# Optimization experiments

Hardware: AMD Instinct MI355X
Metric: run time of the kernel (lower is better)

## Reference

```python
import jax, jax.numpy as jnp
import numpy as np

B, N, D, H, WIN = 8, 4096, 768, 8, 8
HD = D // H
FG = N // 2 + 1
FL = WIN // 2 + 1


def _gelu(x):
    return jax.nn.gelu(x, approximate=False)


def _cgelu(z):
    # magnitude-based complex GELU: z * gelu(|z|) / (|z| + 1e-6)
    mag = jnp.abs(z)
    return z * (_gelu(mag) / (mag + 1e-6))


def setup_inputs():
    key = jax.random.key(0)
    ks = jax.random.split(key, 8)

    def w(k, shape):
        return jax.random.normal(k, shape, dtype=jnp.float32) * 0.02

    return {
        "x": jax.random.normal(ks[0], (B, N, D), dtype=jnp.float32),
        "ln_w": jnp.ones((D,), jnp.float32),
        "ln_b": jnp.zeros((D,), jnp.float32),
        "bf_g": jnp.ones((H, FG, 1), jnp.float32),
        "bb_g": jnp.full((H, FG, 1), -0.1, jnp.float32),
        "bf_l": jnp.ones((H, FL, 1), jnp.float32),
        "bb_l": jnp.full((H, FL, 1), -0.1, jnp.float32),
        "w1g": w(ks[1], (D, D)),
        "b1g": jnp.zeros((D,), jnp.float32),
        "w2g": w(ks[2], (D, H * FG * 2)),
        "b2g": jnp.zeros((H * FG * 2,), jnp.float32),
        "w1l": w(ks[3], (D, D)),
        "b1l": jnp.zeros((D,), jnp.float32),
        "w2l": w(ks[4], (D, H * FL * 2)),
        "b2l": jnp.zeros((H * FL * 2,), jnp.float32),
        "wf1": w(ks[5], (D, D // 2)),
        "bf1": jnp.zeros((D // 2,), jnp.float32),
        "wf2": w(ks[6], (D // 2, H)),
        "bf2": jnp.zeros((H,), jnp.float32),
    }


def reference(x, ln_w, ln_b, bf_g, bb_g, bf_l, bb_l, w1g, b1g, w2g, b2g,
              w1l, b1l, w2l, b2l, wf1, bf1, wf2, bf2):
    # pre-norm (LayerNorm, eps=1e-5)
    mu = jnp.mean(x, axis=-1, keepdims=True)
    var = jnp.mean((x - mu) ** 2, axis=-1, keepdims=True)
    xn = (x - mu) / jnp.sqrt(var + 1e-5) * ln_w + ln_b
    xh = xn.reshape(B, N, H, HD).transpose(0, 2, 1, 3)  # (B,H,N,HD)
    ctx = xn.mean(axis=1)  # (B,D)

    # ---- global branch: Hann-windowed rFFT over full sequence ----
    ag = (_gelu(ctx @ w1g + b1g) @ w2g + b2g).reshape(B, H, FG, 2)
    hann_g = jnp.hanning(N).astype(x.dtype)[None, None, :, None]
    Ff = jnp.fft.rfft(xh * hann_g, axis=2, norm="ortho")  # (B,H,FG,HD) complex
    eff_f = bf_g[None] * (1.0 + ag[..., 0:1])
    eff_b = bb_g[None] + ag[..., 1:2]
    x_global = jnp.fft.irfft(_cgelu(Ff * eff_f + eff_b), n=N, axis=2, norm="ortho")

    al = (_gelu(ctx @ w1l + b1l) @ w2l + b2l).reshape(B, H, FL, 2)
    nw = N // WIN
    hann_l = jnp.hanning(WIN).astype(x.dtype)[None, None, None, :, None]
    xw = xh.reshape(B, H, nw, WIN, HD) * hann_l
    Fl_fft = jnp.fft.rfft(xw, axis=3, norm="ortho")  # (B,H,nw,FL,HD)
    eff_fl = bf_l[None, :, None] * (1.0 + al[:, :, None, :, 0:1])
    eff_bl = bb_l[None, :, None] + al[:, :, None, :, 1:2]
    x_local = jnp.fft.irfft(_cgelu(Fl_fft * eff_fl + eff_bl), n=WIN, axis=3,
                            norm="ortho").reshape(B, H, N, HD)

    # ---- fusion gate ----
    alpha = jax.nn.sigmoid(_gelu(ctx @ wf1 + bf1) @ wf2 + bf2).reshape(B, H, 1, 1)
    fused = alpha * x_global + (1.0 - alpha) * x_local
    return x + fused.transpose(0, 2, 1, 3).reshape(B, N, D)
```

## Files before the change

### kernel.cpp

```cpp
#include <hip/hip_runtime.h>
#include <math.h>

#define B_ 8
#define N_ 4096
#define D_ 768
#define H_ 8
#define HD_ 96
#define FG_ 2049
#define TWO_PI 6.283185307179586476925f
#define PAD(i) ((i) + ((i) >> 5))

__device__ __forceinline__ float gelu_f(float x) {
    return 0.5f * x * (1.0f + erff(x * 0.7071067811865475f));
}

__global__ void k_init(const float* __restrict__ b2g, const float* __restrict__ b2l,
                       float2* __restrict__ twg, float* __restrict__ hanng,
                       float* __restrict__ ctx, float* __restrict__ ag,
                       float* __restrict__ al) {
    int i = blockIdx.x * 256 + threadIdx.x;
    if (i < 2048) {
        float s, c;
        sincosf(-TWO_PI * (float)i / 4096.0f, &s, &c);
        twg[i] = make_float2(c, s);
    }
    if (i < 4096) hanng[i] = 0.5f - 0.5f * cosf(TWO_PI * (float)i / 4095.0f);
    if (i < B_ * D_) ctx[i] = 0.f;
    const int CG = H_ * FG_ * 2;
    if (i < CG) {
        float v = b2g[i];
        for (int b = 0; b < B_; ++b) ag[(size_t)b * CG + i] = v;
    } else if (i < CG + 80) {
        int cc = i - CG;
        float v = b2l[cc];
        for (int b = 0; b < B_; ++b) al[b * 80 + cc] = v;
    }
}

__global__ __launch_bounds__(256) void k_stats(const float* __restrict__ x,
                                               float* __restrict__ mu,
                                               float* __restrict__ rstd) {
    int row = blockIdx.x * 4 + (threadIdx.x >> 6);
    int lane = threadIdx.x & 63;
    const float4* xr = (const float4*)(x + (size_t)row * D_);
    float4 a = xr[lane], b = xr[lane + 64], c = xr[lane + 128];
    float s = a.x + a.y + a.z + a.w + b.x + b.y + b.z + b.w + c.x + c.y + c.z + c.w;
    #pragma unroll
    for (int o = 32; o > 0; o >>= 1) s += __shfl_xor(s, o);
    float m = s * (1.0f / 768.0f);
    float v = 0.f, d;
    d = a.x - m; v += d * d; d = a.y - m; v += d * d;
    d = a.z - m; v += d * d; d = a.w - m; v += d * d;
    d = b.x - m; v += d * d; d = b.y - m; v += d * d;
    d = b.z - m; v += d * d; d = b.w - m; v += d * d;
    d = c.x - m; v += d * d; d = c.y - m; v += d * d;
    d = c.z - m; v += d * d; d = c.w - m; v += d * d;
    #pragma unroll
    for (int o = 32; o > 0; o >>= 1) v += __shfl_xor(v, o);
    if (lane == 0) {
        mu[row] = m;
        rstd[row] = rsqrtf(v * (1.0f / 768.0f) + 1e-5f);
    }
}

__global__ __launch_bounds__(256) void k_lnT(const float* __restrict__ x,
                                             const float* __restrict__ mu,
                                             const float* __restrict__ rstd,
                                             const float* __restrict__ lw,
                                             const float* __restrict__ lb,
                                             float* __restrict__ xt,
                                             float* __restrict__ ctx) {
    __shared__ float tile[64][65];
    __shared__ float csum[4][64];
    int d0 = blockIdx.x * 64, n0 = blockIdx.y * 64, b = blockIdx.z;
    int c = threadIdx.x & 63, r4 = threadIdx.x >> 6;
    float w = lw[d0 + c], bias = lb[d0 + c];
    float partial = 0.f;
    #pragma unroll
    for (int q = 0; q < 16; ++q) {
        int r = r4 * 16 + q;
        int row = b * N_ + n0 + r;
        float v = (x[(size_t)row * D_ + d0 + c] - mu[row]) * rstd[row] * w + bias;
        tile[r][c] = v;
        partial += v;
    }
    csum[r4][c] = partial;
    __syncthreads();
    if (r4 == 0)
        atomicAdd(ctx + b * D_ + d0 + c,
                  (csum[0][c] + csum[1][c] + csum[2][c] + csum[3][c]) * (1.0f / 4096.0f));
    #pragma unroll
    for (int q = 0; q < 16; ++q) {
        int r = r4 * 16 + q;
        xt[((size_t)b * D_ + d0 + r) * N_ + n0 + c] = tile[c][r];
    }
}

__global__ void k_mlp1(const float* __restrict__ ctx,
                       const float* __restrict__ w1g, const float* __restrict__ b1g,
                       const float* __restrict__ w1l, const float* __restrict__ b1l,
                       const float* __restrict__ wf1, const float* __restrict__ bf1,
                       float* __restrict__ h1g, float* __restrict__ h1l, float* __restrict__ hf) {
    __shared__ float cl[B_ * D_];
    for (int i = threadIdx.x; i < B_ * D_; i += 256) cl[i] = ctx[i];
    __syncthreads();
    int c = blockIdx.x * 256 + threadIdx.x;
    if (c >= 1920) return;
    const float *w, *bias; float* out; int ncol, cc;
    if (c < 768)      { w = w1g; bias = b1g; out = h1g; ncol = 768; cc = c; }
    else if (c < 1536){ w = w1l; bias = b1l; out = h1l; ncol = 768; cc = c - 768; }
    else              { w = wf1; bias = bf1; out = hf;  ncol = 384; cc = c - 1536; }
    float acc[B_];
    #pragma unroll
    for (int b = 0; b < B_; ++b) acc[b] = 0.f;
    for (int d = 0; d < 768; ++d) {
        float wv = w[(size_t)d * ncol + cc];
        #pragma unroll
        for (int b = 0; b < B_; ++b) acc[b] += cl[b * 768 + d] * wv;
    }
    float bv = bias[cc];
    for (int b = 0; b < B_; ++b) out[b * ncol + cc] = gelu_f(acc[b] + bv);
}

__global__ void k_mlp2(const float* __restrict__ h1g, const float* __restrict__ h1l,
                       const float* __restrict__ hf,
                       const float* __restrict__ w2g, const float* __restrict__ w2l,
                       const float* __restrict__ wf2, const float* __restrict__ bf2,
                       float* __restrict__ ag, float* __restrict__ al, float* __restrict__ gate) {
    int kc = blockIdx.y;
    int d0 = kc * 96;
    __shared__ float lg[B_ * 96];
    __shared__ float ll[B_ * 96];
    for (int i = threadIdx.x; i < B_ * 96; i += 256) {
        int bb = i / 96, dd = i % 96;
        lg[i] = h1g[bb * 768 + d0 + dd];
        ll[i] = h1l[bb * 768 + d0 + dd];
    }
    __syncthreads();
    int c = blockIdx.x * 256 + threadIdx.x;
    const int CG = H_ * FG_ * 2;
    float acc[B_];
    #pragma unroll
    for (int b = 0; b < B_; ++b) acc[b] = 0.f;
    if (c < CG) {
        for (int d = 0; d < 96; ++d) {
            float wv = w2g[(size_t)(d0 + d) * CG + c];
            #pragma unroll
            for (int b = 0; b < B_; ++b) acc[b] += lg[b * 96 + d] * wv;
        }
        for (int b = 0; b < B_; ++b) atomicAdd(ag + (size_t)b * CG + c, acc[b]);
    } else if (c < CG + 80) {
        int cc = c - CG;
        for (int d = 0; d < 96; ++d) {
            float wv = w2l[(d0 + d) * 80 + cc];
            #pragma unroll
            for (int b = 0; b < B_; ++b) acc[b] += ll[b * 96 + d] * wv;
        }
        for (int b = 0; b < B_; ++b) atomicAdd(al + b * 80 + cc, acc[b]);
    } else if (c < CG + 88 && kc == 0) {
        int cc = c - CG - 80;
        for (int d = 0; d < 384; ++d) {
            float wv = wf2[d * 8 + cc];
            #pragma unroll
            for (int b = 0; b < B_; ++b) acc[b] += hf[b * 384 + d] * wv;
        }
        for (int b = 0; b < B_; ++b)
            gate[b * 8 + cc] = 1.0f / (1.0f + expf(-(acc[b] + bf2[cc])));
    }
}

__device__ __forceinline__ void fft_pass(float2* z, const float2* tw4,
                                         const float2* __restrict__ twg,
                                         int t, float sign) {
    float2 v[16];
    #pragma unroll
    for (int i = 0; i < 16; ++i) v[i] = z[PAD(t * 16 + i)];
    const float TC[8] = {1.f, 0.92387953251f, 0.70710678119f, 0.38268343236f,
                         0.f, -0.38268343236f, -0.70710678119f, -0.92387953251f};
    const float TS[8] = {0.f, -0.38268343236f, -0.70710678119f, -0.92387953251f,
                         -1.f, -0.92387953251f, -0.70710678119f, -0.38268343236f};
    #pragma unroll
    for (int s = 1; s <= 4; ++s) {
        int half = 1 << (s - 1);
        #pragma unroll
        for (int u = 0; u < 8; ++u) {
            int lg = u >> (s - 1), pos = u & (half - 1);
            int i1 = (lg << s) + pos, i2 = i1 + half;
            int m = pos << (4 - s);
            float wr = TC[m], wi = sign * TS[m];
            float2 a = v[i1], bb = v[i2];
            float tr = bb.x * wr - bb.y * wi;
            float ti = bb.x * wi + bb.y * wr;
            v[i1] = make_float2(a.x + tr, a.y + ti);
            v[i2] = make_float2(a.x - tr, a.y - ti);
        }
    }
    #pragma unroll
    for (int i = 0; i < 16; ++i) z[PAD(t * 16 + i)] = v[i];
    __syncthreads();
    for (int s = 5; s <= 10; ++s) {
        int half = 1 << (s - 1);
        int sh = 12 - s;
        #pragma unroll
        for (int u = 0; u < 8; ++u) {
            int j = t + (u << 8);
            int grp = j >> (s - 1);
            int pos = j & (half - 1);
            int i1 = (grp << s) + pos;
            int p1 = PAD(i1), p2 = PAD(i1 + half);
            float2 w = tw4[PAD(pos << (sh - 2))];
            float wi = sign * w.y;
            float2 a = z[p1], bb = z[p2];
            float tr = bb.x * w.x - bb.y * wi;
            float ti = bb.x * wi + bb.y * w.x;
            z[p1] = make_float2(a.x + tr, a.y + ti);
            z[p2] = make_float2(a.x - tr, a.y - ti);
        }
        __syncthreads();
    }
    for (int s = 11; s <= 12; ++s) {
        int half = 1 << (s - 1);
        int sh = 12 - s;
        #pragma unroll
        for (int u = 0; u < 8; ++u) {
            int j = t + (u << 8);
            int grp = j >> (s - 1);
            int pos = j & (half - 1);
            int i1 = (grp << s) + pos;
            int p1 = PAD(i1), p2 = PAD(i1 + half);
            float2 w = twg[pos << sh];
            float wi = sign * w.y;
            float2 a = z[p1], bb = z[p2];
            float tr = bb.x * w.x - bb.y * wi;
            float ti = bb.x * wi + bb.y * w.x;
            z[p1] = make_float2(a.x + tr, a.y + ti);
            z[p2] = make_float2(a.x - tr, a.y - ti);
        }
        __syncthreads();
    }
}

__global__ __launch_bounds__(256) void k_spectral(
        const float* __restrict__ xt,
        const float* __restrict__ ag,
        const float* __restrict__ al,
        const float* __restrict__ gate,
        const float* __restrict__ bf_g, const float* __restrict__ bb_g,
        const float* __restrict__ bf_l, const float* __restrict__ bb_l,
        const float2* __restrict__ twg, const float* __restrict__ hanng,
        float* __restrict__ fused)
{
    __shared__ float2 z[4224];
    __shared__ float2 tw4[528];
    int line0 = blockIdx.x * 2;
    int d0 = line0 % 768, b = line0 / 768;
    int h = d0 / HD_;
    int t = threadIdx.x;

    for (int m = t; m < 512; m += 256) tw4[PAD(m)] = twg[4 * m];

    const float* src0 = xt + (size_t)line0 * N_;
    const float* src1 = src0 + N_;
    float raw0[16], raw1[16];
    #pragma unroll
    for (int q = 0; q < 4; ++q) {
        float4 v0 = ((const float4*)src0)[t * 4 + q];
        float4 v1 = ((const float4*)src1)[t * 4 + q];
        raw0[q * 4 + 0] = v0.x; raw0[q * 4 + 1] = v0.y;
        raw0[q * 4 + 2] = v0.z; raw0[q * 4 + 3] = v0.w;
        raw1[q * 4 + 0] = v1.x; raw1[q * 4 + 1] = v1.y;
        raw1[q * 4 + 2] = v1.z; raw1[q * 4 + 3] = v1.w;
    }
    #pragma unroll
    for (int q = 0; q < 4; ++q) {
        float4 hw = ((const float4*)hanng)[t * 4 + q];
        int nb = t * 16 + q * 4;
        int r0 = PAD((int)(__brev((unsigned)(nb + 0)) >> 20));
        int r1 = PAD((int)(__brev((unsigned)(nb + 1)) >> 20));
        int r2 = PAD((int)(__brev((unsigned)(nb + 2)) >> 20));
        int r3 = PAD((int)(__brev((unsigned)(nb + 3)) >> 20));
        z[r0] = make_float2(raw0[q * 4 + 0] * hw.x, raw1[q * 4 + 0] * hw.x);
        z[r1] = make_float2(raw0[q * 4 + 1] * hw.y, raw1[q * 4 + 1] * hw.y);
        z[r2] = make_float2(raw0[q * 4 + 2] * hw.z, raw1[q * 4 + 2] * hw.z);
        z[r3] = make_float2(raw0[q * 4 + 3] * hw.w, raw1[q * 4 + 3] * hw.w);
    }

    float alc = gate[b * 8 + h];
    const float* alb = al + b * 80;
    float effl_f[5], effl_b[5];
    #pragma unroll
    for (int f = 0; f < 5; ++f) {
        int idx = h * 5 + f;
        effl_f[f] = bf_l[idx] * (1.0f + alb[idx * 2]);
        effl_b[f] = bb_l[idx] + alb[idx * 2 + 1];
    }
    const float s8 = 0.3535533905932738f;
    const float c7 = 0.7071067811865476f;
    const float cosT[8] = {1.f, c7, 0.f, -c7, -1.f, -c7, 0.f, c7};
    const float sinT[8] = {0.f, c7, 1.f, c7, 0.f, -c7, -1.f, -c7};
    const float hl[8] = {0.f, 0.18825510f, 0.61126047f, 0.95048444f,
                         0.95048444f, 0.61126047f, 0.18825510f, 0.f};
    float xl0[16], xl1[16];
    #pragma unroll
    for (int ln = 0; ln < 2; ++ln) {
        float* rawp = ln ? raw1 : raw0;
        float* xlp  = ln ? xl1 : xl0;
        #pragma unroll
        for (int w2 = 0; w2 < 2; ++w2) {
            float xw[8];
            #pragma unroll
            for (int j = 0; j < 8; ++j) xw[j] = rawp[w2 * 8 + j] * hl[j];
            float Yr[5], Yi[5];
            #pragma unroll
            for (int f = 0; f < 5; ++f) {
                float fr = 0.f, fi = 0.f;
                #pragma unroll
                for (int j = 0; j < 8; ++j) {
                    int k8 = (f * j) & 7;
                    fr += xw[j] * cosT[k8];
                    fi -= xw[j] * sinT[k8];
                }
                fr *= s8; fi *= s8;
                float zr = fr * effl_f[f] + effl_b[f];
                float zi = fi * effl_f[f];
                float mag = sqrtf(zr * zr + zi * zi);
                float g = gelu_f(mag) / (mag + 1e-6f);
                Yr[f] = zr * g; Yi[f] = zi * g;
            }
            #pragma unroll
            for (int j = 0; j < 8; ++j) {
                float acc = Yr[0] + Yr[4] * ((j & 1) ? -1.f : 1.f);
                #pragma unroll
                for (int f = 1; f < 4; ++f) {
                    int k8 = (f * j) & 7;
                    acc += 2.f * (Yr[f] * cosT[k8] - Yi[f] * sinT[k8]);
                }
                xlp[w2 * 8 + j] = acc * s8;
            }
        }
    }

    __syncthreads();
    fft_pass(z, tw4, twg, t, 1.0f);

    const float inv64 = 1.0f / 64.0f;
    const float* agb = ag + (size_t)b * 32784;
    for (int k = t; k < 2048; k += 256) {
        int km = (4096 - k) & 4095;
        int pk = PAD(k), pm = PAD(km);
        float2 Z = z[pk], Z2 = z[pm];
        float X0r = 0.5f * (Z.x + Z2.x), X0i = 0.5f * (Z.y - Z2.y);
        float X1r = 0.5f * (Z.y + Z2.y), X1i = -0.5f * (Z.x - Z2.x);
        int idx = h * FG_ + k;
        float efff = bf_g[idx] * (1.0f + agb[idx * 2]);
        float effb = bb_g[idx] + agb[idx * 2 + 1];
        float z0r = X0r * inv64 * efff + effb, z0i = X0i * inv64 * efff;
        float m0 = sqrtf(z0r * z0r + z0i * z0i);
        float g0 = gelu_f(m0) / (m0 + 1e-6f);
        float Y0r = z0r * g0, Y0i = z0i * g0;
        float z1r = X1r * inv64 * efff + effb, z1i = X1i * inv64 * efff;
        float m1 = sqrtf(z1r * z1r + z1i * z1i);
        float g1 = gelu_f(m1) / (m1 + 1e-6f);
        float Y1r = z1r * g1, Y1i = z1i * g1;
        z[pk] = make_float2(Y0r - Y1i, Y0i + Y1r);
        if (k) z[pm] = make_float2(Y0r + Y1i, Y1r - Y0i);
    }
    if (t == 0) {
        int pk = PAD(2048);
        float2 Z = z[pk];
        int idx = h * FG_ + 2048;
        float efff = bf_g[idx] * (1.0f + agb[idx * 2]);
        float effb = bb_g[idx] + agb[idx * 2 + 1];
        float z0r = Z.x * inv64 * efff + effb;
        float m0 = fabsf(z0r);
        float Y0r = z0r * (gelu_f(m0) / (m0 + 1e-6f));
        float z1r = Z.y * inv64 * efff + effb;
        float m1 = fabsf(z1r);
        float Y1r = z1r * (gelu_f(m1) / (m1 + 1e-6f));
        z[pk] = make_float2(Y0r, Y1r);
    }
    __syncthreads();
    for (int n = t; n < 4096; n += 256) {
        int r = (int)(__brev((unsigned)n) >> 20);
        if (r > n) {
            int pn = PAD(n), pr = PAD(r);
            float2 a = z[pn]; z[pn] = z[pr]; z[pr] = a;
        }
    }
    __syncthreads();
    fft_pass(z, tw4, twg, t, -1.0f);

    float* dst0 = fused + (size_t)line0 * N_;
    float* dst1 = dst0 + N_;
    float one_m = 1.0f - alc;
    #pragma unroll
    for (int q = 0; q < 4; ++q) {
        int base = t * 16 + q * 4;
        float2 za = z[PAD(base + 0)], zb = z[PAD(base + 1)];
        float2 zc = z[PAD(base + 2)], zd = z[PAD(base + 3)];
        float4 v0 = make_float4(alc * za.x * inv64 + one_m * xl0[q * 4 + 0],
                                alc * zb.x * inv64 + one_m * xl0[q * 4 + 1],
                                alc * zc.x * inv64 + one_m * xl0[q * 4 + 2],
                                alc * zd.x * inv64 + one_m * xl0[q * 4 + 3]);
        float4 v1 = make_float4(alc * za.y * inv64 + one_m * xl1[q * 4 + 0],
                                alc * zb.y * inv64 + one_m * xl1[q * 4 + 1],
                                alc * zc.y * inv64 + one_m * xl1[q * 4 + 2],
                                alc * zd.y * inv64 + one_m * xl1[q * 4 + 3]);
        ((float4*)dst0)[t * 4 + q] = v0;
        ((float4*)dst1)[t * 4 + q] = v1;
    }
}

__global__ void k_addout(const float* __restrict__ fused, const float* __restrict__ x,
                         float* __restrict__ out) {
    __shared__ float tile[64][65];
    int d0 = blockIdx.x * 64, n0 = blockIdx.y * 64, b = blockIdx.z;
    int c = threadIdx.x & 63, r4 = threadIdx.x >> 6;
    for (int q = 0; q < 16; ++q) {
        int r = r4 * 16 + q;
        tile[r][c] = fused[((size_t)b * D_ + d0 + r) * N_ + n0 + c];
    }
    __syncthreads();
    for (int q = 0; q < 16; ++q) {
        int r = r4 * 16 + q;
        size_t o = ((size_t)b * N_ + n0 + r) * D_ + d0 + c;
        out[o] = x[o] + tile[c][r];
    }
}

extern "C" void kernel_launch(void* const* d_in, const int* in_sizes, int n_in,
                              void* d_out, int out_size, void* d_ws, size_t ws_size,
                              hipStream_t stream) {
    const float* x    = (const float*)d_in[0];
    const float* ln_w = (const float*)d_in[1];
    const float* ln_b = (const float*)d_in[2];
    const float* bf_g = (const float*)d_in[3];
    const float* bb_g = (const float*)d_in[4];
    const float* bf_l = (const float*)d_in[5];
    const float* bb_l = (const float*)d_in[6];
    const float* w1g  = (const float*)d_in[7];
    const float* b1g  = (const float*)d_in[8];
    const float* w2g  = (const float*)d_in[9];
    const float* b2g  = (const float*)d_in[10];
    const float* w1l  = (const float*)d_in[11];
    const float* b1l  = (const float*)d_in[12];
    const float* w2l  = (const float*)d_in[13];
    const float* b2l  = (const float*)d_in[14];
    const float* wf1  = (const float*)d_in[15];
    const float* bf1  = (const float*)d_in[16];
    const float* wf2  = (const float*)d_in[17];
    const float* bf2  = (const float*)d_in[18];
    float* out = (float*)d_out;

    char* ws = (char*)d_ws;
    const size_t big = (size_t)B_ * D_ * N_ * sizeof(float);
    float* XT  = (float*)ws; ws += big;
    float* FU  = (float*)ws; ws += big;
    float* ctx = (float*)ws; ws += (size_t)B_ * D_ * 4;
    float* h1g = (float*)ws; ws += (size_t)B_ * 768 * 4;
    float* h1l = (float*)ws; ws += (size_t)B_ * 768 * 4;
    float* hf  = (float*)ws; ws += (size_t)B_ * 384 * 4;
    float* ag  = (float*)ws; ws += (size_t)B_ * 32784 * 4;
    float* alb = (float*)ws; ws += (size_t)B_ * 80 * 4;
    float* gat = (float*)ws; ws += (size_t)B_ * 8 * 4;
    float2* twg = (float2*)ws; ws += 2048 * sizeof(float2);
    float* hanng = (float*)ws; ws += 4096 * sizeof(float);
    float* mu   = FU;
    float* rstd = FU + 32768;

    k_init<<<129, 256, 0, stream>>>(b2g, b2l, twg, hanng, ctx, ag, alb);
    k_stats<<<8192, 256, 0, stream>>>(x, mu, rstd);
    k_lnT<<<dim3(12, 64, 8), 256, 0, stream>>>(x, mu, rstd, ln_w, ln_b, XT, ctx);
    k_mlp1<<<8, 256, 0, stream>>>(ctx, w1g, b1g, w1l, b1l, wf1, bf1, h1g, h1l, hf);
    k_mlp2<<<dim3(129, 8), 256, 0, stream>>>(h1g, h1l, hf, w2g, w2l, wf2, bf2, ag, alb, gat);
    k_spectral<<<B_ * D_ / 2, 256, 0, stream>>>(XT, ag, alb, gat, bf_g, bb_g, bf_l, bb_l,
                                                twg, hanng, FU);
    k_addout<<<dim3(12, 64, 8), 256, 0, stream>>>(FU, x, out);
}
```

Before: 681.9 us.

## Replace radix-2 FFT with radix-4 DIF/DIT pair and fast erf approximation

New measurement: 610.7 us. 10.4% less time.

```diff
diff --git a/kernel.cpp b/kernel.cpp
--- a/kernel.cpp
+++ b/kernel.cpp
@@ -10,8 +10,22 @@
 #define TWO_PI 6.283185307179586476925f
 #define PAD(i) ((i) + ((i) >> 5))
 
+__device__ __forceinline__ float erf_fast(float x) {
+    float ax = fabsf(x);
+    float t = __builtin_amdgcn_rcpf(fmaf(0.3275911f, ax, 1.0f));
+    float p = fmaf(fmaf(fmaf(fmaf(1.061405429f, t, -1.453152027f), t, 1.421413741f),
+                        t, -0.284496736f), t, 0.254829592f) * t;
+    float r = 1.0f - p * __expf(-ax * ax);
+    return copysignf(r, x);
+}
+
 __device__ __forceinline__ float gelu_f(float x) {
-    return 0.5f * x * (1.0f + erff(x * 0.7071067811865475f));
+    return 0.5f * x * (1.0f + erf_fast(x * 0.7071067811865475f));
+}
+
+__device__ __forceinline__ int rev4_12(int x) {
+    int r = (int)(__brev((unsigned)x) >> 20);
+    return ((r & 0x555) << 1) | ((r >> 1) & 0x555);
 }
 
 __global__ void k_init(const float* __restrict__ b2g, const float* __restrict__ b2l,
@@ -169,74 +183,120 @@
     }
 }
 
-__device__ __forceinline__ void fft_pass(float2* z, const float2* tw4,
-                                         const float2* __restrict__ twg,
-                                         int t, float sign) {
-    float2 v[16];
-    #pragma unroll
-    for (int i = 0; i < 16; ++i) v[i] = z[PAD(t * 16 + i)];
-    const float TC[8] = {1.f, 0.92387953251f, 0.70710678119f, 0.38268343236f,
-                         0.f, -0.38268343236f, -0.70710678119f, -0.92387953251f};
-    const float TS[8] = {0.f, -0.38268343236f, -0.70710678119f, -0.92387953251f,
-                         -1.f, -0.92387953251f, -0.70710678119f, -0.38268343236f};
-    #pragma unroll
-    for (int s = 1; s <= 4; ++s) {
-        int half = 1 << (s - 1);
-        #pragma unroll
-        for (int u = 0; u < 8; ++u) {
-            int lg = u >> (s - 1), pos = u & (half - 1);
-            int i1 = (lg << s) + pos, i2 = i1 + half;
-            int m = pos << (4 - s);
-            float wr = TC[m], wi = sign * TS[m];
-            float2 a = v[i1], bb = v[i2];
-            float tr = bb.x * wr - bb.y * wi;
-            float ti = bb.x * wi + bb.y * wr;
-            v[i1] = make_float2(a.x + tr, a.y + ti);
-            v[i2] = make_float2(a.x - tr, a.y - ti);
-        }
-    }
-    #pragma unroll
-    for (int i = 0; i < 16; ++i) z[PAD(t * 16 + i)] = v[i];
-    __syncthreads();
-    for (int s = 5; s <= 10; ++s) {
-        int half = 1 << (s - 1);
-        int sh = 12 - s;
-        #pragma unroll
-        for (int u = 0; u < 8; ++u) {
-            int j = t + (u << 8);
-            int grp = j >> (s - 1);
-            int pos = j & (half - 1);
-            int i1 = (grp << s) + pos;
-            int p1 = PAD(i1), p2 = PAD(i1 + half);
-            float2 w = tw4[PAD(pos << (sh - 2))];
-            float wi = sign * w.y;
-            float2 a = z[p1], bb = z[p2];
-            float tr = bb.x * w.x - bb.y * wi;
-            float ti = bb.x * wi + bb.y * w.x;
-            z[p1] = make_float2(a.x + tr, a.y + ti);
-            z[p2] = make_float2(a.x - tr, a.y - ti);
-        }
-        __syncthreads();
-    }
-    for (int s = 11; s <= 12; ++s) {
-        int half = 1 << (s - 1);
-        int sh = 12 - s;
-        #pragma unroll
-        for (int u = 0; u < 8; ++u) {
-            int j = t + (u << 8);
-            int grp = j >> (s - 1);
-            int pos = j & (half - 1);
-            int i1 = (grp << s) + pos;
-            int p1 = PAD(i1), p2 = PAD(i1 + half);
-            float2 w = twg[pos << sh];
-            float wi = sign * w.y;
-            float2 a = z[p1], bb = z[p2];
-            float tr = bb.x * w.x - bb.y * wi;
-            float ti = bb.x * wi + bb.y * w.x;
-            z[p1] = make_float2(a.x + tr, a.y + ti);
-            z[p2] = make_float2(a.x - tr, a.y - ti);
-        }
-        __syncthreads();
+template<int LQ>
+__device__ __forceinline__ void dif_stage(float2* z, const float2* __restrict__ twg, int t) {
+    const int Q = 1 << LQ;
+    #pragma unroll
+    for (int u = 0; u < 4; ++u) {
+        int j = t + (u << 8);
+        int pos = j & (Q - 1);
+        int i0 = ((j >> LQ) << (LQ + 2)) + pos;
+        int p0 = PAD(i0), p1 = PAD(i0 + Q), p2 = PAD(i0 + 2 * Q), p3 = PAD(i0 + 3 * Q);
+        float2 a = z[p0], bq = z[p1], c = z[p2], d = z[p3];
+        float t0x = a.x + c.x,  t0y = a.y + c.y;
+        float t1x = a.x - c.x,  t1y = a.y - c.y;
+        float t2x = bq.x + d.x, t2y = bq.y + d.y;
+        float t3x = bq.x - d.x, t3y = bq.y - d.y;
+        float2 w1 = twg[pos << (10 - LQ)];
+        float2 w2 = make_float2(w1.x * w1.x - w1.y * w1.y, 2.f * w1.x * w1.y);
+        float2 w3 = make_float2(w1.x * w2.x - w1.y * w2.y, w1.x * w2.y + w1.y * w2.x);
+        z[p0] = make_float2(t0x + t2x, t0y + t2y);
+        float y1x = t1x + t3y, y1y = t1y - t3x;
+        z[p1] = make_float2(y1x * w1.x - y1y * w1.y, y1x * w1.y + y1y * w1.x);
+        float y2x = t0x - t2x, y2y = t0y - t2y;
+        z[p2] = make_float2(y2x * w2.x - y2y * w2.y, y2x * w2.y + y2y * w2.x);
+        float y3x = t1x - t3y, y3y = t1y + t3x;
+        z[p3] = make_float2(y3x * w3.x - y3y * w3.y, y3x * w3.y + y3y * w3.x);
+    }
+}
+
+template<int LQ>
+__device__ __forceinline__ void dit_stage(float2* z, const float2* __restrict__ twg, int t) {
+    const int Q = 1 << LQ;
+    #pragma unroll
+    for (int u = 0; u < 4; ++u) {
+        int j = t + (u << 8);
+        int pos = j & (Q - 1);
+        int i0 = ((j >> LQ) << (LQ + 2)) + pos;
+        int p0 = PAD(i0), p1 = PAD(i0 + Q), p2 = PAD(i0 + 2 * Q), p3 = PAD(i0 + 3 * Q);
+        float2 a = z[p0], bq = z[p1], c = z[p2], d = z[p3];
+        float2 w1 = twg[pos << (10 - LQ)];
+        w1.y = -w1.y;
+        float2 w2 = make_float2(w1.x * w1.x - w1.y * w1.y, 2.f * w1.x * w1.y);
+        float2 w3 = make_float2(w1.x * w2.x - w1.y * w2.y, w1.x * w2.y + w1.y * w2.x);
+        float2 bh = make_float2(bq.x * w1.x - bq.y * w1.y, bq.x * w1.y + bq.y * w1.x);
+        float2 ch = make_float2(c.x * w2.x - c.y * w2.y, c.x * w2.y + c.y * w2.x);
+        float2 dh = make_float2(d.x * w3.x - d.y * w3.y, d.x * w3.y + d.y * w3.x);
+        float t0x = a.x + ch.x,  t0y = a.y + ch.y;
+        float t1x = a.x - ch.x,  t1y = a.y - ch.y;
+        float t2x = bh.x + dh.x, t2y = bh.y + dh.y;
+        float t3x = bh.x - dh.x, t3y = bh.y - dh.y;
+        z[p0] = make_float2(t0x + t2x, t0y + t2y);
+        z[p1] = make_float2(t1x - t3y, t1y + t3x);
+        z[p2] = make_float2(t0x - t2x, t0y - t2y);
+        z[p3] = make_float2(t1x + t3y, t1y - t3x);
+    }
+}
+
+#define W16C_INIT {1.f, 0.9238795325f, 0.7071067812f, 0.3826834324f, 0.f, \
+                   -0.3826834324f, -0.7071067812f, -0.9238795325f, -1.f, -0.9238795325f}
+#define W16S_INIT {0.f, -0.3826834324f, -0.7071067812f, -0.9238795325f, -1.f, \
+                   -0.9238795325f, -0.7071067812f, -0.3826834324f, 0.f, 0.3826834324f}
+
+__device__ __forceinline__ void fwd16(float2* v) {
+    const float WC[10] = W16C_INIT;
+    const float WS[10] = W16S_INIT;
+    #pragma unroll
+    for (int n0 = 0; n0 < 4; ++n0) {
+        float2 a = v[n0], b = v[n0 + 4], c = v[n0 + 8], d = v[n0 + 12];
+        float t0x = a.x + c.x, t0y = a.y + c.y, t1x = a.x - c.x, t1y = a.y - c.y;
+        float t2x = b.x + d.x, t2y = b.y + d.y, t3x = b.x - d.x, t3y = b.y - d.y;
+        v[n0] = make_float2(t0x + t2x, t0y + t2y);
+        float y1x = t1x + t3y, y1y = t1y - t3x;
+        float y2x = t0x - t2x, y2y = t0y - t2y;
+        float y3x = t1x - t3y, y3y = t1y + t3x;
+        v[n0 + 4]  = make_float2(y1x * WC[n0] - y1y * WS[n0], y1x * WS[n0] + y1y * WC[n0]);
+        v[n0 + 8]  = make_float2(y2x * WC[2*n0] - y2y * WS[2*n0], y2x * WS[2*n0] + y2y * WC[2*n0]);
+        v[n0 + 12] = make_float2(y3x * WC[3*n0] - y3y * WS[3*n0], y3x * WS[3*n0] + y3y * WC[3*n0]);
+    }
+    #pragma unroll
+    for (int g = 0; g < 4; ++g) {
+        float2 a = v[4*g], b = v[4*g+1], c = v[4*g+2], d = v[4*g+3];
+        float t0x = a.x + c.x, t0y = a.y + c.y, t1x = a.x - c.x, t1y = a.y - c.y;
+        float t2x = b.x + d.x, t2y = b.y + d.y, t3x = b.x - d.x, t3y = b.y - d.y;
+        v[4*g]   = make_float2(t0x + t2x, t0y + t2y);
+        v[4*g+1] = make_float2(t1x + t3y, t1y - t3x);
+        v[4*g+2] = make_float2(t0x - t2x, t0y - t2y);
+        v[4*g+3] = make_float2(t1x - t3y, t1y + t3x);
+    }
+}
+
+__device__ __forceinline__ void inv16(float2* v) {
+    const float WC[10] = W16C_INIT;
+    const float WS[10] = W16S_INIT;
+    #pragma unroll
+    for (int g = 0; g < 4; ++g) {
+        float2 a = v[4*g], b = v[4*g+1], c = v[4*g+2], d = v[4*g+3];
+        float t0x = a.x + c.x, t0y = a.y + c.y, t1x = a.x - c.x, t1y = a.y - c.y;
+        float t2x = b.x + d.x, t2y = b.y + d.y, t3x = b.x - d.x, t3y = b.y - d.y;
+        v[4*g]   = make_float2(t0x + t2x, t0y + t2y);
+        v[4*g+1] = make_float2(t1x - t3y, t1y + t3x);
+        v[4*g+2] = make_float2(t0x - t2x, t0y - t2y);
+        v[4*g+3] = make_float2(t1x + t3y, t1y - t3x);
+    }
+    #pragma unroll
+    for (int n0 = 0; n0 < 4; ++n0) {
+        float2 a = v[n0];
+        float2 b0 = v[n0 + 4], c0 = v[n0 + 8], dd = v[n0 + 12];
+        float2 b = make_float2(b0.x * WC[n0] + b0.y * WS[n0], b0.y * WC[n0] - b0.x * WS[n0]);
+        float2 c = make_float2(c0.x * WC[2*n0] + c0.y * WS[2*n0], c0.y * WC[2*n0] - c0.x * WS[2*n0]);
+        float2 d = make_float2(dd.x * WC[3*n0] + dd.y * WS[3*n0], dd.y * WC[3*n0] - dd.x * WS[3*n0]);
+        float t0x = a.x + c.x, t0y = a.y + c.y, t1x = a.x - c.x, t1y = a.y - c.y;
+        float t2x = b.x + d.x, t2y = b.y + d.y, t3x = b.x - d.x, t3y = b.y - d.y;
+        v[n0]      = make_float2(t0x + t2x, t0y + t2y);
+        v[n0 + 4]  = make_float2(t1x - t3y, t1y + t3x);
+        v[n0 + 8]  = make_float2(t0x - t2x, t0y - t2y);
+        v[n0 + 12] = make_float2(t1x + t3y, t1y - t3x);
     }
 }
 
@@ -251,13 +311,10 @@
         float* __restrict__ fused)
 {
     __shared__ float2 z[4224];
-    __shared__ float2 tw4[528];
     int line0 = blockIdx.x * 2;
     int d0 = line0 % 768, b = line0 / 768;
     int h = d0 / HD_;
     int t = threadIdx.x;
-
-    for (int m = t; m < 512; m += 256) tw4[PAD(m)] = twg[4 * m];
 
     const float* src0 = xt + (size_t)line0 * N_;
     const float* src1 = src0 + N_;
@@ -275,14 +332,10 @@
     for (int q = 0; q < 4; ++q) {
         float4 hw = ((const float4*)hanng)[t * 4 + q];
         int nb = t * 16 + q * 4;
-        int r0 = PAD((int)(__brev((unsigned)(nb + 0)) >> 20));
-        int r1 = PAD((int)(__brev((unsigned)(nb + 1)) >> 20));
-        int r2 = PAD((int)(__brev((unsigned)(nb + 2)) >> 20));
-        int r3 = PAD((int)(__brev((unsigned)(nb + 3)) >> 20));
-        z[r0] = make_float2(raw0[q * 4 + 0] * hw.x, raw1[q * 4 + 0] * hw.x);
-        z[r1] = make_float2(raw0[q * 4 + 1] * hw.y, raw1[q * 4 + 1] * hw.y);
-        z[r2] = make_float2(raw0[q * 4 + 2] * hw.z, raw1[q * 4 + 2] * hw.z);
-        z[r3] = make_float2(raw0[q * 4 + 3] * hw.w, raw1[q * 4 + 3] * hw.w);
+        z[PAD(nb + 0)] = make_float2(raw0[q * 4 + 0] * hw.x, raw1[q * 4 + 0] * hw.x);
+        z[PAD(nb + 1)] = make_float2(raw0[q * 4 + 1] * hw.y, raw1[q * 4 + 1] * hw.y);
+        z[PAD(nb + 2)] = make_float2(raw0[q * 4 + 2] * hw.z, raw1[q * 4 + 2] * hw.z);
+        z[PAD(nb + 3)] = make_float2(raw0[q * 4 + 3] * hw.w, raw1[q * 4 + 3] * hw.w);
     }
 
     float alc = gate[b * 8 + h];
@@ -324,7 +377,7 @@
                 float zr = fr * effl_f[f] + effl_b[f];
                 float zi = fi * effl_f[f];
                 float mag = sqrtf(zr * zr + zi * zi);
-                float g = gelu_f(mag) / (mag + 1e-6f);
+                float g = gelu_f(mag) * __builtin_amdgcn_rcpf(mag + 1e-6f);
                 Yr[f] = zr * g; Yi[f] = zi * g;
             }
             #pragma unroll
@@ -341,13 +394,25 @@
     }
 
     __syncthreads();
-    fft_pass(z, tw4, twg, t, 1.0f);
+    dif_stage<10>(z, twg, t); __syncthreads();
+    dif_stage<8>(z, twg, t);  __syncthreads();
+    dif_stage<6>(z, twg, t);  __syncthreads();
+    dif_stage<4>(z, twg, t);  __syncthreads();
+    {
+        float2 v[16];
+        #pragma unroll
+        for (int i = 0; i < 16; ++i) v[i] = z[PAD(t * 16 + i)];
+        fwd16(v);
+        #pragma unroll
+        for (int i = 0; i < 16; ++i) z[PAD(t * 16 + i)] = v[i];
+    }
+    __syncthreads();
 
     const float inv64 = 1.0f / 64.0f;
     const float* agb = ag + (size_t)b * 32784;
     for (int k = t; k < 2048; k += 256) {
         int km = (4096 - k) & 4095;
-        int pk = PAD(k), pm = PAD(km);
+        int pk = PAD(rev4_12(k)), pm = PAD(rev4_12(km));
         float2 Z = z[pk], Z2 = z[pm];
         float X0r = 0.5f * (Z.x + Z2.x), X0i = 0.5f * (Z.y - Z2.y);
         float X1r = 0.5f * (Z.y + Z2.y), X1i = -0.5f * (Z.x - Z2.x);
@@ -356,39 +421,44 @@
         float effb = bb_g[idx] + agb[idx * 2 + 1];
         float z0r = X0r * inv64 * efff + effb, z0i = X0i * inv64 * efff;
         float m0 = sqrtf(z0r * z0r + z0i * z0i);
-        float g0 = gelu_f(m0) / (m0 + 1e-6f);
+        float g0 = gelu_f(m0) * __builtin_amdgcn_rcpf(m0 + 1e-6f);
         float Y0r = z0r * g0, Y0i = z0i * g0;
         float z1r = X1r * inv64 * efff + effb, z1i = X1i * inv64 * efff;
         float m1 = sqrtf(z1r * z1r + z1i * z1i);
-        float g1 = gelu_f(m1) / (m1 + 1e-6f);
+        float g1 = gelu_f(m1) * __builtin_amdgcn_rcpf(m1 + 1e-6f);
         float Y1r = z1r * g1, Y1i = z1i * g1;
         z[pk] = make_float2(Y0r - Y1i, Y0i + Y1r);
         if (k) z[pm] = make_float2(Y0r + Y1i, Y1r - Y0i);
     }
     if (t == 0) {
-        int pk = PAD(2048);
+        int pk = PAD(rev4_12(2048));
         float2 Z = z[pk];
         int idx = h * FG_ + 2048;
         float efff = bf_g[idx] * (1.0f + agb[idx * 2]);
         float effb = bb_g[idx] + agb[idx * 2 + 1];
         float z0r = Z.x * inv64 * efff + effb;
         float m0 = fabsf(z0r);
-        float Y0r = z0r * (gelu_f(m0) / (m0 + 1e-6f));
+        float Y0r = z0r * (gelu_f(m0) * __builtin_amdgcn_rcpf(m0 + 1e-6f));
         float z1r = Z.y * inv64 * efff + effb;
         float m1 = fabsf(z1r);
-        float Y1r = z1r * (gelu_f(m1) / (m1 + 1e-6f));
+        float Y1r = z1r * (gelu_f(m1) * __builtin_amdgcn_rcpf(m1 + 1e-6f));
         z[pk] = make_float2(Y0r, Y1r);
     }
     __syncthreads();
-    for (int n = t; n < 4096; n += 256) {
-        int r = (int)(__brev((unsigned)n) >> 20);
-        if (r > n) {
-            int pn = PAD(n), pr = PAD(r);
-            float2 a = z[pn]; z[pn] = z[pr]; z[pr] = a;
-        }
-    }
-    __syncthreads();
-    fft_pass(z, tw4, twg, t, -1.0f);
+
+    {
+        float2 v[16];
+        #pragma unroll
+        for (int i = 0; i < 16; ++i) v[i] = z[PAD(t * 16 + i)];
+        inv16(v);
+        #pragma unroll
+        for (int i = 0; i < 16; ++i) z[PAD(t * 16 + i)] = v[i];
+    }
+    __syncthreads();
+    dit_stage<4>(z, twg, t);  __syncthreads();
+    dit_stage<6>(z, twg, t);  __syncthreads();
+    dit_stage<8>(z, twg, t);  __syncthreads();
+    dit_stage<10>(z, twg, t); __syncthreads();
 
     float* dst0 = fused + (size_t)line0 * N_;
     float* dst1 = dst0 + N_;
```
